# Optimization experiments

Measured on AMD Instinct MI355X. Metric: run time of the kernel, lower is better.

## Reference

```python
import jax, jax.numpy as jnp
import numpy as np

B, HIST, PRED = 16, 336, 48
S = HIST + PRED                      # 384 = max_seq_length
H, NL, NH, FF = 768, 12, 12, 3072    # default BertConfig
SA_NH = 16                           # attention_heads arg for the extra SelfAttention
V = 40000                            # num_location_ids
NE = 8                               # num_experts
D_DAY, D_TIME, D_DOW, D_WD, D_LOC = 64, 64, 64, 32, 256
D_IN = D_DAY + D_TIME + D_DOW + D_WD + D_LOC + 1  # 481


def _ln(x, g, b, eps):
    m = jnp.mean(x, -1, keepdims=True)
    v = jnp.mean(jnp.square(x - m), -1, keepdims=True)
    return (x - m) * jax.lax.rsqrt(v + eps) * g + b


def _mha(x, qW, qb, kW, kb, vW, vb, nh):
    b_, s_, h_ = x.shape
    hd = h_ // nh
    q = (x @ qW + qb).reshape(b_, s_, nh, hd)
    k = (x @ kW + kb).reshape(b_, s_, nh, hd)
    v = (x @ vW + vb).reshape(b_, s_, nh, hd)
    scores = jnp.einsum('bqhd,bkhd->bhqk', q, k) / jnp.sqrt(jnp.float32(hd))
    probs = jax.nn.softmax(scores, axis=-1)
    return jnp.einsum('bhqk,bkhd->bqhd', probs, v).reshape(b_, s_, h_)


FLOAT_NAMES = ['day_emb', 'time_emb', 'dow_emb', 'wd_emb', 'loc_emb',
               'ln_in_g', 'ln_in_b', 'inp_W', 'inp_b', 'res_W', 'res_b',
               'sa_qW', 'sa_qb', 'sa_kW', 'sa_kb', 'sa_vW', 'sa_vb', 'sa_oW', 'sa_ob', 'sa_lng', 'sa_lnb',
               'pos_emb', 'tt_emb', 'be_lng', 'be_lnb',
               'bqW', 'bqb', 'bkW', 'bkb', 'bvW', 'bvb', 'boW', 'bob', 'balng', 'balnb',
               'bf1W', 'bf1b', 'bf2W', 'bf2b', 'bflng', 'bflnb',
               'moe_W', 'moe_b', 'gate_W', 'gate_b', 'out_W', 'out_b']


def _forward(floats, ints):
    (day_emb, time_emb, dow_emb, wd_emb, loc_emb,
     ln_in_g, ln_in_b, inp_W, inp_b, res_W, res_b,
     sa_qW, sa_qb, sa_kW, sa_kb, sa_vW, sa_vb, sa_oW, sa_ob, sa_lng, sa_lnb,
     pos_emb, tt_emb, be_lng, be_lnb,
     bqW, bqb, bkW, bkb, bvW, bvb, boW, bob, balng, balnb,
     bf1W, bf1b, bf2W, bf2b, bflng, bflnb,
     moe_W, moe_b, gate_W, gate_b, out_W, out_b) = floats
    isf, hloc, psf = ints

    def feat(f):
        return (day_emb[f[:, :, 0]], time_emb[f[:, :, 1]], dow_emb[f[:, :, 3]],
                wd_emb[f[:, :, 4]], f[:, :, 5].astype(jnp.float32)[..., None])
    hd_, ht_, hw_, hwd_, hdl = feat(isf)
    hist = jnp.concatenate([hd_, ht_, hw_, hwd_, hdl, loc_emb[hloc]], -1)
    fd_, ft_, fw_, fwd_, fdl = feat(psf)
    fut_loc = jnp.zeros((psf.shape[0], psf.shape[1], D_LOC), jnp.float32)  # unknown future locations
    fut = jnp.concatenate([fd_, ft_, fw_, fwd_, fdl, fut_loc], -1)
    x = jnp.concatenate([hist, fut], 1)            # [B,S,481]
    x = _ln(x, ln_in_g, ln_in_b, 1e-5)             # layer_norm on raw features (dropout = identity in eval)
    proj = x @ inp_W + inp_b                       # input_projection -> [B,S,768]
    res = x @ res_W + res_b                        # residual_fc -> [B,S,768]

    # extra SelfAttention block (16 heads) with post-LN residual
    ctx = _mha(proj, sa_qW, sa_qb, sa_kW, sa_kb, sa_vW, sa_vb, SA_NH)
    h = _ln(ctx @ sa_oW + sa_ob + proj, sa_lng, sa_lnb, 1e-5)

    # BERT encoder (inputs_embeds path): add position + token_type(0) embeddings, then 12 post-LN layers
    h = _ln(h + pos_emb[None] + tt_emb, be_lng, be_lnb, 1e-12)
    for i in range(NL):
        ctx = _mha(h, bqW[i], bqb[i], bkW[i], bkb[i], bvW[i], bvb[i], NH)
        a = _ln(ctx @ boW[i] + bob[i] + h, balng[i], balnb[i], 1e-12)
        ff = jax.nn.gelu(a @ bf1W[i] + bf1b[i], approximate=False) @ bf2W[i] + bf2b[i]
        h = _ln(ff + a, bflng[i], bflnb[i], 1e-12)

    # dense soft-MoE: every expert runs on every token, softmax-gated sum
    xf = h.reshape(-1, H)                                                 # [B*S, H]
    eo = jax.nn.gelu(jnp.einsum('nd,edh->neh', xf, moe_W) + moe_b[None], approximate=False)
    gp = jax.nn.softmax(xf @ gate_W + gate_b, axis=-1)                     # [B*S, E]
    moe_out = jnp.einsum('ne,neh->nh', gp, eo).reshape(h.shape)

    logits = (moe_out + res) @ out_W + out_b                               # [B,S,V]
    return logits[:, HIST:, :]                                             # predictions for future slots


def setup_inputs() -> dict:
    key = jax.random.key(0)
    ctr = [0]
    def nk():
        ctr[0] += 1
        return jax.random.fold_in(key, ctr[0])
    def nrm(shape, s=0.02):
        return jax.random.normal(nk(), shape, jnp.float32) * s
    p = {}
    p['input_seq_feature'] = jax.random.randint(nk(), (B, HIST, 6), 0, 2)
    p['historical_locations'] = jax.random.randint(nk(), (B, HIST), 0, V)
    p['predict_seq_feature'] = jax.random.randint(nk(), (B, PRED, 6), 0, 2)
    p['day_emb'] = nrm((75, D_DAY)); p['time_emb'] = nrm((48, D_TIME))
    p['dow_emb'] = nrm((7, D_DOW)); p['wd_emb'] = nrm((2, D_WD)); p['loc_emb'] = nrm((V, D_LOC))
    p['ln_in_g'] = jnp.ones((D_IN,), jnp.float32); p['ln_in_b'] = jnp.zeros((D_IN,), jnp.float32)
    p['inp_W'] = nrm((D_IN, H)); p['inp_b'] = jnp.zeros((H,), jnp.float32)
    p['res_W'] = nrm((D_IN, H)); p['res_b'] = jnp.zeros((H,), jnp.float32)
    for n in ['sa_qW', 'sa_kW', 'sa_vW', 'sa_oW']:
        p[n] = nrm((H, H))
    for n in ['sa_qb', 'sa_kb', 'sa_vb', 'sa_ob']:
        p[n] = jnp.zeros((H,), jnp.float32)
    p['sa_lng'] = jnp.ones((H,), jnp.float32); p['sa_lnb'] = jnp.zeros((H,), jnp.float32)
    p['pos_emb'] = nrm((S, H)); p['tt_emb'] = nrm((H,))
    p['be_lng'] = jnp.ones((H,), jnp.float32); p['be_lnb'] = jnp.zeros((H,), jnp.float32)
    for n in ['bqW', 'bkW', 'bvW', 'boW']:
        p[n] = nrm((NL, H, H))
    for n in ['bqb', 'bkb', 'bvb', 'bob']:
        p[n] = jnp.zeros((NL, H), jnp.float32)
    p['balng'] = jnp.ones((NL, H), jnp.float32); p['balnb'] = jnp.zeros((NL, H), jnp.float32)
    p['bf1W'] = nrm((NL, H, FF)); p['bf1b'] = jnp.zeros((NL, FF), jnp.float32)
    p['bf2W'] = nrm((NL, FF, H)); p['bf2b'] = jnp.zeros((NL, H), jnp.float32)
    p['bflng'] = jnp.ones((NL, H), jnp.float32); p['bflnb'] = jnp.zeros((NL, H), jnp.float32)
    p['moe_W'] = nrm((NE, H, H)); p['moe_b'] = jnp.zeros((NE, H), jnp.float32)
    p['gate_W'] = nrm((H, NE)); p['gate_b'] = jnp.zeros((NE,), jnp.float32)
    p['out_W'] = nrm((H, V)); p['out_b'] = jnp.zeros((V,), jnp.float32)
    return p


def reference(input_seq_feature, historical_locations, predict_seq_feature,
              day_emb, time_emb, dow_emb, wd_emb, loc_emb,
              ln_in_g, ln_in_b, inp_W, inp_b, res_W, res_b,
              sa_qW, sa_qb, sa_kW, sa_kb, sa_vW, sa_vb, sa_oW, sa_ob, sa_lng, sa_lnb,
              pos_emb, tt_emb, be_lng, be_lnb,
              bqW, bqb, bkW, bkb, bvW, bvb, boW, bob, balng, balnb,
              bf1W, bf1b, bf2W, bf2b, bflng, bflnb,
              moe_W, moe_b, gate_W, gate_b, out_W, out_b):
    floats = (day_emb, time_emb, dow_emb, wd_emb, loc_emb,
              ln_in_g, ln_in_b, inp_W, inp_b, res_W, res_b,
              sa_qW, sa_qb, sa_kW, sa_kb, sa_vW, sa_vb, sa_oW, sa_ob, sa_lng, sa_lnb,
              pos_emb, tt_emb, be_lng, be_lnb,
              bqW, bqb, bkW, bkb, bvW, bvb, boW, bob, balng, balnb,
              bf1W, bf1b, bf2W, bf2b, bflng, bflnb,
              moe_W, moe_b, gate_W, gate_b, out_W, out_b)
    ints = (input_seq_feature, historical_locations, predict_seq_feature)
    return _forward(floats, ints)
```

## Files before the change

### kernel.cpp

```cpp
#include <hip/hip_runtime.h>
#include <cstddef>
#include <math.h>

#define BB 16
#define HIST 336
#define PRED 48
#define SS 384
#define HH 768
#define NL 12
#define FF_ 3072
#define DIN 481
#define DINP 512
#define NE_ 8
#define VV 40000
#define VVP 40064

typedef __attribute__((ext_vector_type(8))) short short8;
typedef __attribute__((ext_vector_type(4))) float f32x4;
struct short4v { short x, y, z, w; };

__device__ __forceinline__ short f2bf(float f) {
    union { float f; unsigned u; } v; v.f = f;
    unsigned r = v.u + 0x7fff + ((v.u >> 16) & 1);
    return (short)(r >> 16);
}

using gvoid_t = const __attribute__((address_space(1))) void;
using svoid_t = __attribute__((address_space(3))) void;

template<int OP>
__global__ __launch_bounds__(256)
void gemm_bf16(const short* __restrict__ A, const short* __restrict__ Bt,
               const float* __restrict__ bias, const float* __restrict__ bias2,
               const float* __restrict__ bias3,
               void* __restrict__ Cout, void* __restrict__ Cout2,
               int Kp, int M, int ldc)
{
    __shared__ short As[2][128 * 64];
    __shared__ short Bs[2][128 * 64];
    const int tid  = threadIdx.x;
    const int lane = tid & 63;
    const int w    = tid >> 6;
    const int wr = w >> 1, wc = w & 1;
    const int lrow = lane & 15, lgrp = lane >> 4;
    const size_t rowBase = (size_t)blockIdx.y * 128;
    const size_t colBase = (size_t)blockIdx.x * 128;

    f32x4 acc[4][4];
    #pragma unroll
    for (int i = 0; i < 4; ++i)
        #pragma unroll
        for (int j = 0; j < 4; ++j)
            acc[i][j] = f32x4{0.f, 0.f, 0.f, 0.f};

    const int nkt = Kp >> 6;

    auto stage = [&](int buf, int kt) {
        const short* Ab = A  + rowBase * Kp + (size_t)kt * 64;
        const short* Bb = Bt + colBase * Kp + (size_t)kt * 64;
        #pragma unroll
        for (int c = 0; c < 4; ++c) {
            const int sidx = (w * 4 + c) * 64 + lane;
            const int r = sidx >> 3, sl = sidx & 7;
            const int sseg = sl ^ (r & 7);
            __builtin_amdgcn_global_load_lds(
                (gvoid_t*)(Ab + (size_t)r * Kp + sseg * 8),
                (svoid_t*)&As[buf][(w * 4 + c) * 512], 16, 0, 0);
            __builtin_amdgcn_global_load_lds(
                (gvoid_t*)(Bb + (size_t)r * Kp + sseg * 8),
                (svoid_t*)&Bs[buf][(w * 4 + c) * 512], 16, 0, 0);
        }
    };

    int cur = 0;
    stage(0, 0);
    __syncthreads();
    for (int kt = 0; kt < nkt; ++kt) {
        if (kt + 1 < nkt) stage(cur ^ 1, kt + 1);
        const short* as = As[cur];
        const short* bs = Bs[cur];
        #pragma unroll
        for (int kk = 0; kk < 2; ++kk) {
            short8 aF[4], bF[4];
            #pragma unroll
            for (int mi = 0; mi < 4; ++mi) {
                const int r = wr * 64 + mi * 16 + lrow;
                const int seg = (kk * 4 + lgrp) ^ (r & 7);
                aF[mi] = *(const short8*)&as[r * 64 + seg * 8];
            }
            #pragma unroll
            for (int ni = 0; ni < 4; ++ni) {
                const int r = wc * 64 + ni * 16 + lrow;
                const int seg = (kk * 4 + lgrp) ^ (r & 7);
                bF[ni] = *(const short8*)&bs[r * 64 + seg * 8];
            }
            #pragma unroll
            for (int mi = 0; mi < 4; ++mi)
                #pragma unroll
                for (int ni = 0; ni < 4; ++ni)
                    acc[mi][ni] = __builtin_amdgcn_mfma_f32_16x16x32_bf16(
                        aF[mi], bF[ni], acc[mi][ni], 0, 0, 0);
        }
        __syncthreads();
        cur ^= 1;
    }

    #pragma unroll
    for (int mi = 0; mi < 4; ++mi) {
        #pragma unroll
        for (int ni = 0; ni < 4; ++ni) {
            const int col = (int)colBase + wc * 64 + ni * 16 + lrow;
            if (col >= M) continue;
            const float* bp = bias; int bc = col;
            if (bias2 && col >= HH) {
                if (col < 2 * HH) { bp = bias2; bc = col - HH; }
                else              { bp = bias3; bc = col - 2 * HH; }
            }
            const float bz = bp[bc];
            #pragma unroll
            for (int j = 0; j < 4; ++j) {
                const size_t row = rowBase + wr * 64 + mi * 16 + lgrp * 4 + j;
                float v = acc[mi][ni][j] + bz;
                if (OP == 1 || OP == 4)
                    v = 0.5f * v * (1.f + erff(v * 0.70710678118654752f));
                if (OP == 4 || OP == 5) ((short*)Cout)[row * ldc + col] = f2bf(v);
                else                    ((float*)Cout)[row * ldc + col] = v;
                if (OP == 6)            ((short*)Cout2)[row * ldc + col] = f2bf(v);
            }
        }
    }
}

template<int HD>
__global__ __launch_bounds__(256)
void attn_mfma(const short* __restrict__ Qg, const short* __restrict__ Kg,
               const short* __restrict__ Vg, short* __restrict__ Og,
               int nh, int ldq, int ldo, float scale)
{
    constexpr int NI = HD / 16;
    constexpr int SEGS = HD / 8;
    __shared__ short Qs[64 * 64];
    __shared__ short Ks[64 * 64];
    __shared__ short Vt[64 * 72];
    __shared__ short Ps[4][16 * 80];
    int idx = blockIdx.x;
    const int qt = idx % 6; idx /= 6;
    const int h = idx % nh; idx /= nh;
    const int b = idx;
    const int tid = threadIdx.x;
    const int lane = tid & 63;
    const int w = tid >> 6;
    const int lrow = lane & 15, lgrp = lane >> 4;

    const short* Qbase = Qg + ((size_t)(b * SS + qt * 64)) * ldq + h * HD;
    #pragma unroll
    for (int t = 0; t < 2; ++t) {
        const int i = tid + t * 256;
        const int r = i >> 3, sg = i & 7;
        short8 v = {0, 0, 0, 0, 0, 0, 0, 0};
        if (sg < SEGS) v = *(const short8*)(Qbase + (size_t)r * ldq + sg * 8);
        *(short8*)&Qs[r * 64 + (sg ^ (r & 7)) * 8] = v;
    }

    float m_[4], l_[4];
    f32x4 o_[NI];
    #pragma unroll
    for (int j = 0; j < 4; ++j) { m_[j] = -1e30f; l_[j] = 0.f; }
    #pragma unroll
    for (int ni = 0; ni < NI; ++ni) o_[ni] = f32x4{0.f, 0.f, 0.f, 0.f};

    for (int kt = 0; kt < 6; ++kt) {
        const short* Kb2 = Kg + ((size_t)(b * SS + kt * 64)) * ldq + h * HD;
        const short* Vb2 = Vg + ((size_t)(b * SS + kt * 64)) * ldq + h * HD;
        __syncthreads();
        #pragma unroll
        for (int c = 0; c < 2; ++c) {
            const int r = (w * 2 + c) * 8 + (lane >> 3);
            const int sg = (lane & 7) ^ (r & 7);
            __builtin_amdgcn_global_load_lds(
                (gvoid_t*)(Kb2 + (size_t)r * ldq + sg * 8),
                (svoid_t*)&Ks[(w * 2 + c) * 512], 16, 0, 0);
        }
        for (int i = tid; i < 64 * SEGS; i += 256) {
            const int k = i & 63, sg = i >> 6;
            short8 v = *(const short8*)(Vb2 + (size_t)k * ldq + sg * 8);
            #pragma unroll
            for (int j2 = 0; j2 < 8; ++j2)
                Vt[(sg * 8 + j2) * 72 + k] = v[j2];
        }
        __syncthreads();

        f32x4 s[4];
        #pragma unroll
        for (int ni = 0; ni < 4; ++ni) s[ni] = f32x4{0.f, 0.f, 0.f, 0.f};
        #pragma unroll
        for (int kk = 0; kk < 2; ++kk) {
            const int ra = w * 16 + lrow;
            const short8 aF = *(const short8*)&Qs[ra * 64 + ((kk * 4 + lgrp) ^ (ra & 7)) * 8];
            #pragma unroll
            for (int ni = 0; ni < 4; ++ni) {
                const int rb = ni * 16 + lrow;
                const short8 bF = *(const short8*)&Ks[rb * 64 + ((kk * 4 + lgrp) ^ (rb & 7)) * 8];
                s[ni] = __builtin_amdgcn_mfma_f32_16x16x32_bf16(aF, bF, s[ni], 0, 0, 0);
            }
        }
        #pragma unroll
        for (int ni = 0; ni < 4; ++ni)
            #pragma unroll
            for (int j = 0; j < 4; ++j) s[ni][j] *= scale;

        #pragma unroll
        for (int j = 0; j < 4; ++j) {
            float tm = fmaxf(fmaxf(s[0][j], s[1][j]), fmaxf(s[2][j], s[3][j]));
            #pragma unroll
            for (int d = 1; d < 16; d <<= 1) tm = fmaxf(tm, __shfl_xor(tm, d));
            const float mn = fmaxf(m_[j], tm);
            const float r2 = __expf(m_[j] - mn);
            float p[4], ps = 0.f;
            #pragma unroll
            for (int ni = 0; ni < 4; ++ni) { p[ni] = __expf(s[ni][j] - mn); ps += p[ni]; }
            #pragma unroll
            for (int d = 1; d < 16; d <<= 1) ps += __shfl_xor(ps, d);
            l_[j] = l_[j] * r2 + ps;
            m_[j] = mn;
            #pragma unroll
            for (int ni = 0; ni < NI; ++ni) o_[ni][j] *= r2;
            #pragma unroll
            for (int ni = 0; ni < 4; ++ni)
                Ps[w][(lgrp * 4 + j) * 80 + ni * 16 + lrow] = f2bf(p[ni]);
        }

        #pragma unroll
        for (int kk = 0; kk < 2; ++kk) {
            const short8 aP = *(const short8*)&Ps[w][lrow * 80 + kk * 32 + lgrp * 8];
            #pragma unroll
            for (int ni = 0; ni < NI; ++ni) {
                const int d0 = ni * 16 + lrow;
                const short8 bV = *(const short8*)&Vt[d0 * 72 + (kk * 4 + lgrp) * 8];
                o_[ni] = __builtin_amdgcn_mfma_f32_16x16x32_bf16(aP, bV, o_[ni], 0, 0, 0);
            }
        }
    }

    const size_t orow0 = (size_t)(b * SS + qt * 64 + w * 16);
    #pragma unroll
    for (int j = 0; j < 4; ++j) {
        const float inv = 1.f / l_[j];
        #pragma unroll
        for (int ni = 0; ni < NI; ++ni)
            Og[(orow0 + lgrp * 4 + j) * ldo + h * HD + ni * 16 + lrow] =
                f2bf(o_[ni][j] * inv);
    }
}

__global__ __launch_bounds__(256)
void transpose_cvt_b(const float* __restrict__ W, short* __restrict__ Wt,
                     int K, int M, int Kp, size_t sStride, size_t dStride)
{
    __shared__ float tile[32][33];
    const float* src = W + blockIdx.z * sStride;
    short* dst = Wt + blockIdx.z * dStride;
    const int m0 = blockIdx.x * 32, k0 = blockIdx.y * 32;
    const int tx = threadIdx.x, ty = threadIdx.y;
    #pragma unroll
    for (int i = 0; i < 4; ++i) {
        int k = k0 + ty + i * 8, m = m0 + tx;
        tile[ty + i * 8][tx] = (k < K && m < M) ? src[(size_t)k * M + m] : 0.f;
    }
    __syncthreads();
    #pragma unroll
    for (int i = 0; i < 4; ++i) {
        int m = m0 + ty + i * 8, k = k0 + tx;
        dst[(size_t)m * Kp + k] = f2bf(tile[tx][ty + i * 8]);
    }
}

__global__ __launch_bounds__(256)
void prep_layer_w(const float* __restrict__ bq, const float* __restrict__ bk,
                  const float* __restrict__ bv, const float* __restrict__ bo,
                  const float* __restrict__ f1, const float* __restrict__ f2,
                  short* __restrict__ qkvT, short* __restrict__ oT,
                  short* __restrict__ f1T, short* __restrict__ f2T)
{
    __shared__ float tile[32][33];
    int id = blockIdx.x;
    const float* src; short* dst; int K, M, tm, tk;
    if (id < 1728) {
        const int mat = id / 576, r = id % 576;
        src = mat == 0 ? bq : (mat == 1 ? bk : bv);
        dst = qkvT + (size_t)mat * HH * HH;
        K = HH; M = HH; tm = r % 24; tk = r / 24;
    } else if (id < 2304) {
        const int r = id - 1728;
        src = bo; dst = oT; K = HH; M = HH; tm = r % 24; tk = r / 24;
    } else if (id < 4608) {
        const int r = id - 2304;
        src = f1; dst = f1T; K = HH; M = FF_; tm = r % 96; tk = r / 96;
    } else {
        const int r = id - 4608;
        src = f2; dst = f2T; K = FF_; M = HH; tm = r % 24; tk = r / 24;
    }
    const int m0 = tm * 32, k0 = tk * 32;
    const int tx = threadIdx.x & 31, ty = threadIdx.x >> 5;
    #pragma unroll
    for (int i = 0; i < 4; ++i) {
        int k = k0 + ty + i * 8, m = m0 + tx;
        tile[ty + i * 8][tx] = src[(size_t)k * M + m];
    }
    __syncthreads();
    #pragma unroll
    for (int i = 0; i < 4; ++i) {
        int m = m0 + ty + i * 8, k = k0 + tx;
        dst[(size_t)m * K + k] = f2bf(tile[tx][ty + i * 8]);
    }
}

__global__ __launch_bounds__(256)
void cvt_bf16(const float* __restrict__ src, short* __restrict__ dst, int n4)
{
    int i = blockIdx.x * 256 + threadIdx.x;
    if (i >= n4) return;
    float4 v = reinterpret_cast<const float4*>(src)[i];
    short4v o = { f2bf(v.x), f2bf(v.y), f2bf(v.z), f2bf(v.w) };
    reinterpret_cast<short4v*>(dst)[i] = o;
}

__global__ __launch_bounds__(512)
void build_x(const int* __restrict__ isf, const int* __restrict__ hloc,
             const int* __restrict__ psf,
             const float* __restrict__ dayE, const float* __restrict__ timeE,
             const float* __restrict__ dowE, const float* __restrict__ wdE,
             const float* __restrict__ locE,
             const float* __restrict__ g, const float* __restrict__ b2,
             short* __restrict__ xb)
{
    const int tok = blockIdx.x;
    const int b = tok / SS, s = tok % SS;
    const int tid = threadIdx.x;
    __shared__ float red[512];
    const int* f;
    int loc = -1;
    if (s < HIST) { f = isf + (b * HIST + s) * 6; loc = hloc[b * HIST + s]; }
    else          { f = psf + (b * PRED + (s - HIST)) * 6; }
    float val = 0.f;
    if (tid < DIN) {
        int c = tid;
        if      (c < 64)  val = dayE[f[0] * 64 + c];
        else if (c < 128) val = timeE[f[1] * 64 + (c - 64)];
        else if (c < 192) val = dowE[f[3] * 64 + (c - 128)];
        else if (c < 224) val = wdE[f[4] * 32 + (c - 192)];
        else if (c == 224) val = (float)f[5];
        else val = (loc >= 0) ? locE[(size_t)loc * 256 + (c - 225)] : 0.f;
    }
    red[tid] = (tid < DIN) ? val : 0.f;
    __syncthreads();
    for (int o = 256; o > 0; o >>= 1) { if (tid < o) red[tid] += red[tid + o]; __syncthreads(); }
    float mean = red[0] / (float)DIN;
    __syncthreads();
    float d = (tid < DIN) ? (val - mean) : 0.f;
    red[tid] = d * d;
    __syncthreads();
    for (int o = 256; o > 0; o >>= 1) { if (tid < o) red[tid] += red[tid + o]; __syncthreads(); }
    float rstd = rsqrtf(red[0] / (float)DIN + 1e-5f);
    if (tid < DINP)
        xb[(size_t)tok * DINP + tid] =
            (tid < DIN) ? f2bf((val - mean) * rstd * g[tid] + b2[tid]) : (short)0;
}

__global__ __launch_bounds__(256)
void ln768(float* __restrict__ out, short* __restrict__ outb,
           const float* __restrict__ in1, const float* __restrict__ in2,
           const float* __restrict__ pos, const float* __restrict__ tt,
           const float* __restrict__ g, const float* __restrict__ b2,
           float eps)
{
    const int D = HH;
    const int row = blockIdx.x;
    const int s = row % SS;
    __shared__ float buf[HH];
    __shared__ float red[256];
    const int tid = threadIdx.x;
    float partial = 0.f;
    #pragma unroll
    for (int i = 0; i < 3; ++i) {
        int c = tid + i * 256;
        float v = in1[(size_t)row * D + c];
        if (in2) v += in2[(size_t)row * D + c];
        if (pos) v += pos[(size_t)s * D + c];
        if (tt)  v += tt[c];
        buf[c] = v;
        partial += v;
    }
    red[tid] = partial; __syncthreads();
    for (int o = 128; o > 0; o >>= 1) { if (tid < o) red[tid] += red[tid + o]; __syncthreads(); }
    float mean = red[0] / (float)D;
    __syncthreads();
    float p2 = 0.f;
    #pragma unroll
    for (int i = 0; i < 3; ++i) { float d = buf[tid + i * 256] - mean; p2 += d * d; }
    red[tid] = p2; __syncthreads();
    for (int o = 128; o > 0; o >>= 1) { if (tid < o) red[tid] += red[tid + o]; __syncthreads(); }
    float rstd = rsqrtf(red[0] / (float)D + eps);
    #pragma unroll
    for (int i = 0; i < 3; ++i) {
        int c = tid + i * 256;
        float v = (buf[c] - mean) * rstd * g[c] + b2[c];
        out[(size_t)row * D + c] = v;
        if (outb) outb[(size_t)row * D + c] = f2bf(v);
    }
}

__global__ void gather_fut_f32(const float* __restrict__ src, float* __restrict__ dst, int D)
{
    const int r = blockIdx.x;
    const int b = r / PRED, t = r % PRED;
    const int srow = b * SS + HIST + t;
    for (int c = threadIdx.x; c < D; c += blockDim.x)
        dst[(size_t)r * D + c] = src[(size_t)srow * D + c];
}
__global__ void gather_fut_b16(const short* __restrict__ src, short* __restrict__ dst, int D)
{
    const int r = blockIdx.x;
    const int b = r / PRED, t = r % PRED;
    const int srow = b * SS + HIST + t;
    for (int c = threadIdx.x; c < D; c += blockDim.x)
        dst[(size_t)r * D + c] = src[(size_t)srow * D + c];
}

__global__ __launch_bounds__(256)
void gate_kernel(const float* __restrict__ Xf, const float* __restrict__ Wg,
                 const float* __restrict__ bg, float* __restrict__ out)
{
    const int row = blockIdx.x;
    const int tid = threadIdx.x;
    float a[NE_] = {};
    for (int k = tid; k < HH; k += 256) {
        float xv = Xf[(size_t)row * HH + k];
        #pragma unroll
        for (int e = 0; e < NE_; ++e) a[e] = fmaf(xv, Wg[k * NE_ + e], a[e]);
    }
    __shared__ float red[256];
    #pragma unroll
    for (int e = 0; e < NE_; ++e) {
        red[tid] = a[e]; __syncthreads();
        for (int o = 128; o > 0; o >>= 1) { if (tid < o) red[tid] += red[tid + o]; __syncthreads(); }
        if (tid == 0) out[(size_t)row * NE_ + e] = red[0] + bg[e];
        __syncthreads();
    }
}

__global__ void gate_softmax(float* __restrict__ gate)
{
    const int r = blockIdx.x * blockDim.x + threadIdx.x;
    if (r >= BB * PRED) return;
    float* p = gate + (size_t)r * NE_;
    float mx = p[0];
    for (int e = 1; e < NE_; ++e) mx = fmaxf(mx, p[e]);
    float s = 0.f, v[NE_];
    for (int e = 0; e < NE_; ++e) { v[e] = __expf(p[e] - mx); s += v[e]; }
    for (int e = 0; e < NE_; ++e) p[e] = v[e] / s;
}

__global__ __launch_bounds__(256)
void moe_reduce(const float* __restrict__ eo, const float* __restrict__ gp,
                float* __restrict__ futm)
{
    const int row = blockIdx.x;
    float g[NE_];
    #pragma unroll
    for (int e = 0; e < NE_; ++e) g[e] = gp[row * NE_ + e];
    for (int c = threadIdx.x; c < HH; c += 256) {
        float s = futm[(size_t)row * HH + c];
        #pragma unroll
        for (int e = 0; e < NE_; ++e)
            s = fmaf(g[e], eo[(size_t)row * (NE_ * HH) + e * HH + c], s);
        futm[(size_t)row * HH + c] = s;
    }
}

extern "C" void kernel_launch(void* const* d_in, const int* in_sizes, int n_in,
                              void* d_out, int out_size, void* d_ws, size_t ws_size,
                              hipStream_t stream)
{
    const int*   isf   = (const int*)  d_in[0];
    const int*   hloc  = (const int*)  d_in[1];
    const int*   psf   = (const int*)  d_in[2];
    const float* dayE  = (const float*)d_in[3];
    const float* timeE = (const float*)d_in[4];
    const float* dowE  = (const float*)d_in[5];
    const float* wdE   = (const float*)d_in[6];
    const float* locE  = (const float*)d_in[7];
    const float* ln_g  = (const float*)d_in[8];
    const float* ln_b  = (const float*)d_in[9];
    const float* inpW  = (const float*)d_in[10];
    const float* inpB  = (const float*)d_in[11];
    const float* resW  = (const float*)d_in[12];
    const float* resB  = (const float*)d_in[13];
    const float* saqW  = (const float*)d_in[14];
    const float* sakW  = (const float*)d_in[15];
    const float* savW  = (const float*)d_in[16];
    const float* saoW  = (const float*)d_in[17];
    const float* saqB  = (const float*)d_in[18];
    const float* sakB  = (const float*)d_in[19];
    const float* savB  = (const float*)d_in[20];
    const float* saoB  = (const float*)d_in[21];
    const float* salnG = (const float*)d_in[22];
    const float* salnB = (const float*)d_in[23];
    const float* posE  = (const float*)d_in[24];
    const float* ttE   = (const float*)d_in[25];
    const float* belnG = (const float*)d_in[26];
    const float* belnB = (const float*)d_in[27];
    const float* bqW   = (const float*)d_in[28];
    const float* bkW   = (const float*)d_in[29];
    const float* bvW   = (const float*)d_in[30];
    const float* boW   = (const float*)d_in[31];
    const float* bqB   = (const float*)d_in[32];
    const float* bkB   = (const float*)d_in[33];
    const float* bvB   = (const float*)d_in[34];
    const float* boB   = (const float*)d_in[35];
    const float* balnG = (const float*)d_in[36];
    const float* balnB = (const float*)d_in[37];
    const float* bf1W  = (const float*)d_in[38];
    const float* bf1B  = (const float*)d_in[39];
    const float* bf2W  = (const float*)d_in[40];
    const float* bf2B  = (const float*)d_in[41];
    const float* bflnG = (const float*)d_in[42];
    const float* bflnB = (const float*)d_in[43];
    const float* moeW  = (const float*)d_in[44];
    const float* moeB  = (const float*)d_in[45];
    const float* gateW = (const float*)d_in[46];
    const float* gateB = (const float*)d_in[47];
    const float* outW  = (const float*)d_in[48];
    const float* outB  = (const float*)d_in[49];

    const int N6 = BB * SS;
    const int NF = BB * PRED;

    char* base = (char*)d_ws;
    size_t off = 0;
    auto alloc = [&](size_t bytes) -> void* {
        void* p = base + off;
        off = (off + bytes + 255) & ~(size_t)255;
        return p;
    };

    short* xb     = (short*)alloc((size_t)N6 * DINP * 2);
    short* hb     = (short*)alloc((size_t)N6 * HH * 2);
    short* Ob     = (short*)alloc((size_t)N6 * HH * 2);
    short* QKVb   = (short*)alloc((size_t)N6 * 3 * HH * 2);
    float* Cb     = (float*)alloc((size_t)N6 * HH * 4);
    short* ffb    = (short*)alloc((size_t)N6 * FF_ * 2);
    float* Hh     = (float*)alloc((size_t)N6 * HH * 4);
    float* Abuf   = (float*)alloc((size_t)N6 * HH * 4);
    short* inpWt  = (short*)alloc((size_t)HH * DINP * 2);
    short* resWt  = (short*)alloc((size_t)HH * DINP * 2);
    short* saWt   = (short*)alloc((size_t)3 * HH * HH * 2);
    short* saoWt  = (short*)alloc((size_t)HH * HH * 2);
    short* lqkvWt = (short*)alloc((size_t)3 * HH * HH * 2);
    short* loWt   = (short*)alloc((size_t)HH * HH * 2);
    short* lf1Wt  = (short*)alloc((size_t)FF_ * HH * 2);
    short* lf2Wt  = (short*)alloc((size_t)HH * FF_ * 2);
    float* futh   = (float*)alloc((size_t)NF * HH * 4);
    float* futm   = (float*)alloc((size_t)NF * HH * 4);
    float* futg   = (float*)alloc((size_t)NF * NE_ * 4);

    short* outWt = QKVb;
    short* moeWt = outWt + (size_t)VVP * HH;
    short* futhb = moeWt + (size_t)NE_ * HH * HH;
    short* futxb = futhb + (size_t)NF * HH;
    short* futmb = futxb + (size_t)NF * DINP;

    build_x<<<N6, 512, 0, stream>>>(isf, hloc, psf, dayE, timeE, dowE, wdE, locE,
                                    ln_g, ln_b, xb);

    dim3 tb(32, 8);
    transpose_cvt_b<<<dim3(HH/32, DINP/32, 1), tb, 0, stream>>>(inpW, inpWt, DIN, HH, DINP, 0, 0);
    transpose_cvt_b<<<dim3(HH/32, DINP/32, 1), tb, 0, stream>>>(resW, resWt, DIN, HH, DINP, 0, 0);
    transpose_cvt_b<<<dim3(HH/32, HH/32, 1), tb, 0, stream>>>(saqW, saWt,                   HH, HH, HH, 0, 0);
    transpose_cvt_b<<<dim3(HH/32, HH/32, 1), tb, 0, stream>>>(sakW, saWt + (size_t)HH*HH,   HH, HH, HH, 0, 0);
    transpose_cvt_b<<<dim3(HH/32, HH/32, 1), tb, 0, stream>>>(savW, saWt + (size_t)2*HH*HH, HH, HH, HH, 0, 0);
    transpose_cvt_b<<<dim3(HH/32, HH/32, 1), tb, 0, stream>>>(saoW, saoWt, HH, HH, HH, 0, 0);

    gemm_bf16<6><<<dim3(HH/128, N6/128), 256, 0, stream>>>(
        xb, inpWt, inpB, nullptr, nullptr, Abuf, hb, DINP, HH, HH);

    gemm_bf16<5><<<dim3(3*HH/128, N6/128), 256, 0, stream>>>(
        hb, saWt, saqB, sakB, savB, QKVb, nullptr, HH, 3*HH, 3*HH);
    attn_mfma<48><<<BB*16*6, 256, 0, stream>>>(
        QKVb, QKVb + HH, QKVb + 2*HH, Ob, 16, 3*HH, HH, 1.f / sqrtf(48.f));
    gemm_bf16<0><<<dim3(HH/128, N6/128), 256, 0, stream>>>(
        Ob, saoWt, saoB, nullptr, nullptr, Cb, nullptr, HH, HH, HH);
    ln768<<<N6, 256, 0, stream>>>(Hh, nullptr, Cb, Abuf, nullptr, nullptr,
                                  salnG, salnB, 1e-5f);

    ln768<<<N6, 256, 0, stream>>>(Hh, hb, Hh, nullptr, posE, ttE,
                                  belnG, belnB, 1e-12f);

    for (int i = 0; i < NL; ++i) {
        const size_t wo = (size_t)i * HH * HH;
        const size_t bo = (size_t)i * HH;
        prep_layer_w<<<6912, 256, 0, stream>>>(
            bqW + wo, bkW + wo, bvW + wo, boW + wo,
            bf1W + (size_t)i * HH * FF_, bf2W + (size_t)i * FF_ * HH,
            lqkvWt, loWt, lf1Wt, lf2Wt);

        gemm_bf16<5><<<dim3(3*HH/128, N6/128), 256, 0, stream>>>(
            hb, lqkvWt, bqB + bo, bkB + bo, bvB + bo, QKVb, nullptr, HH, 3*HH, 3*HH);
        attn_mfma<64><<<BB*12*6, 256, 0, stream>>>(
            QKVb, QKVb + HH, QKVb + 2*HH, Ob, 12, 3*HH, HH, 0.125f);
        gemm_bf16<0><<<dim3(HH/128, N6/128), 256, 0, stream>>>(
            Ob, loWt, boB + bo, nullptr, nullptr, Cb, nullptr, HH, HH, HH);
        ln768<<<N6, 256, 0, stream>>>(Abuf, hb, Cb, Hh, nullptr, nullptr,
                                      balnG + bo, balnB + bo, 1e-12f);
        gemm_bf16<4><<<dim3(FF_/128, N6/128), 256, 0, stream>>>(
            hb, lf1Wt, bf1B + (size_t)i * FF_, nullptr, nullptr, ffb, nullptr, HH, FF_, FF_);
        gemm_bf16<0><<<dim3(HH/128, N6/128), 256, 0, stream>>>(
            ffb, lf2Wt, bf2B + bo, nullptr, nullptr, Cb, nullptr, FF_, HH, HH);
        ln768<<<N6, 256, 0, stream>>>(Hh, hb, Cb, Abuf, nullptr, nullptr,
                                      bflnG + bo, bflnB + bo, 1e-12f);
    }

    gather_fut_f32<<<NF, 256, 0, stream>>>(Hh, futh, HH);
    gather_fut_b16<<<NF, 256, 0, stream>>>(hb, futhb, HH);
    gather_fut_b16<<<NF, 256, 0, stream>>>(xb, futxb, DINP);

    gemm_bf16<0><<<dim3(HH/128, NF/128), 256, 0, stream>>>(
        futxb, resWt, resB, nullptr, nullptr, futm, nullptr, DINP, HH, HH);

    gate_kernel<<<NF, 256, 0, stream>>>(futh, gateW, gateB, futg);
    gate_softmax<<<3, 256, 0, stream>>>(futg);

    transpose_cvt_b<<<dim3(HH/32, HH/32, NE_), tb, 0, stream>>>(
        moeW, moeWt, HH, HH, HH, (size_t)HH*HH, (size_t)HH*HH);
    gemm_bf16<1><<<dim3(NE_*HH/128, NF/128), 256, 0, stream>>>(
        futhb, moeWt, moeB, nullptr, nullptr, Hh, nullptr, HH, NE_*HH, NE_*HH);
    moe_reduce<<<NF, 256, 0, stream>>>(Hh, futg, futm);

    {
        int n4 = (int)((size_t)NF * HH / 4);
        cvt_bf16<<<(n4 + 255) / 256, 256, 0, stream>>>(futm, futmb, n4);
    }
    transpose_cvt_b<<<dim3(VVP/32, HH/32, 1), tb, 0, stream>>>(
        outW, outWt, HH, VV, HH, 0, 0);
    gemm_bf16<0><<<dim3(VVP/128, NF/128), 256, 0, stream>>>(
        futmb, outWt, outB, nullptr, nullptr, (float*)d_out, nullptr, HH, VV, VV);
}
```

Measured before the change: 3.735 ms.

## Swizzle GEMM blocks across XCDs, raise MFMA priority, warp-per-row layernorm

Adds an optional XCD-aware block remapping to the GEMM. It is enabled only for the MoE GEMM and the large vocabulary output GEMM, so that neighbouring tiles land on the same XCD and share its L2. The attention kernel gets s_setprio raised around its MFMA sections. The layernorm is rewritten to handle one row per wavefront with float4 loads and shuffle reductions, which removes the shared-memory tree reductions and barriers. The changes are small and mostly independent; the swizzle depends on the grid size dividing evenly and only helps if L2 locality was a bottleneck.

```diff
diff --git a/kernel.cpp b/kernel.cpp
--- a/kernel.cpp
+++ b/kernel.cpp
@@ -28,7 +28,7 @@
 using gvoid_t = const __attribute__((address_space(1))) void;
 using svoid_t = __attribute__((address_space(3))) void;
 
-template<int OP>
+template<int OP, bool SWZ>
 __global__ __launch_bounds__(256)
 void gemm_bf16(const short* __restrict__ A, const short* __restrict__ Bt,
                const float* __restrict__ bias, const float* __restrict__ bias2,
@@ -43,8 +43,19 @@
     const int w    = tid >> 6;
     const int wr = w >> 1, wc = w & 1;
     const int lrow = lane & 15, lgrp = lane >> 4;
-    const size_t rowBase = (size_t)blockIdx.y * 128;
-    const size_t colBase = (size_t)blockIdx.x * 128;
+
+    int bx = blockIdx.x, by = blockIdx.y;
+    if (SWZ) {
+        const int nwg = gridDim.x * gridDim.y;
+        const int o = blockIdx.y * gridDim.x + blockIdx.x;
+        const int xcd = o & 7, k = o >> 3;
+        const int q = nwg >> 3, r = nwg & 7;
+        const int nid = (xcd < r ? xcd * (q + 1) : r * (q + 1) + (xcd - r) * q) + k;
+        bx = nid / gridDim.y;
+        by = nid % gridDim.y;
+    }
+    const size_t rowBase = (size_t)by * 128;
+    const size_t colBase = (size_t)bx * 128;
 
     f32x4 acc[4][4];
     #pragma unroll
@@ -193,6 +204,7 @@
         f32x4 s[4];
         #pragma unroll
         for (int ni = 0; ni < 4; ++ni) s[ni] = f32x4{0.f, 0.f, 0.f, 0.f};
+        __builtin_amdgcn_s_setprio(1);
         #pragma unroll
         for (int kk = 0; kk < 2; ++kk) {
             const int ra = w * 16 + lrow;
@@ -204,6 +216,7 @@
                 s[ni] = __builtin_amdgcn_mfma_f32_16x16x32_bf16(aF, bF, s[ni], 0, 0, 0);
             }
         }
+        __builtin_amdgcn_s_setprio(0);
         #pragma unroll
         for (int ni = 0; ni < 4; ++ni)
             #pragma unroll
@@ -230,6 +243,7 @@
                 Ps[w][(lgrp * 4 + j) * 80 + ni * 16 + lrow] = f2bf(p[ni]);
         }
 
+        __builtin_amdgcn_s_setprio(1);
         #pragma unroll
         for (int kk = 0; kk < 2; ++kk) {
             const short8 aP = *(const short8*)&Ps[w][lrow * 80 + kk * 32 + lgrp * 8];
@@ -240,6 +254,7 @@
                 o_[ni] = __builtin_amdgcn_mfma_f32_16x16x32_bf16(aP, bV, o_[ni], 0, 0, 0);
             }
         }
+        __builtin_amdgcn_s_setprio(0);
     }
 
     const size_t orow0 = (size_t)(b * SS + qt * 64 + w * 16);
@@ -368,45 +383,57 @@
 }
 
 __global__ __launch_bounds__(256)
-void ln768(float* __restrict__ out, short* __restrict__ outb,
-           const float* __restrict__ in1, const float* __restrict__ in2,
-           const float* __restrict__ pos, const float* __restrict__ tt,
-           const float* __restrict__ g, const float* __restrict__ b2,
-           float eps)
-{
-    const int D = HH;
-    const int row = blockIdx.x;
+void ln768w(float* __restrict__ out, short* __restrict__ outb,
+            const float* __restrict__ in1, const float* __restrict__ in2,
+            const float* __restrict__ pos, const float* __restrict__ tt,
+            const float* __restrict__ g, const float* __restrict__ b2,
+            float eps)
+{
+    const int w = threadIdx.x >> 6, lane = threadIdx.x & 63;
+    const int row = blockIdx.x * 4 + w;
     const int s = row % SS;
-    __shared__ float buf[HH];
-    __shared__ float red[256];
-    const int tid = threadIdx.x;
+    float4 v[3];
     float partial = 0.f;
     #pragma unroll
     for (int i = 0; i < 3; ++i) {
-        int c = tid + i * 256;
-        float v = in1[(size_t)row * D + c];
-        if (in2) v += in2[(size_t)row * D + c];
-        if (pos) v += pos[(size_t)s * D + c];
-        if (tt)  v += tt[c];
-        buf[c] = v;
-        partial += v;
-    }
-    red[tid] = partial; __syncthreads();
-    for (int o = 128; o > 0; o >>= 1) { if (tid < o) red[tid] += red[tid + o]; __syncthreads(); }
-    float mean = red[0] / (float)D;
-    __syncthreads();
+        const int c = i * 256 + lane * 4;
+        float4 t = *(const float4*)&in1[(size_t)row * HH + c];
+        if (in2) { float4 u = *(const float4*)&in2[(size_t)row * HH + c];
+                   t.x += u.x; t.y += u.y; t.z += u.z; t.w += u.w; }
+        if (pos) { float4 u = *(const float4*)&pos[(size_t)s * HH + c];
+                   t.x += u.x; t.y += u.y; t.z += u.z; t.w += u.w; }
+        if (tt)  { float4 u = *(const float4*)&tt[c];
+                   t.x += u.x; t.y += u.y; t.z += u.z; t.w += u.w; }
+        v[i] = t;
+        partial += t.x + t.y + t.z + t.w;
+    }
+    #pragma unroll
+    for (int d = 1; d < 64; d <<= 1) partial += __shfl_xor(partial, d);
+    const float mean = partial * (1.f / 768.f);
     float p2 = 0.f;
     #pragma unroll
-    for (int i = 0; i < 3; ++i) { float d = buf[tid + i * 256] - mean; p2 += d * d; }
-    red[tid] = p2; __syncthreads();
-    for (int o = 128; o > 0; o >>= 1) { if (tid < o) red[tid] += red[tid + o]; __syncthreads(); }
-    float rstd = rsqrtf(red[0] / (float)D + eps);
-    #pragma unroll
     for (int i = 0; i < 3; ++i) {
-        int c = tid + i * 256;
-        float v = (buf[c] - mean) * rstd * g[c] + b2[c];
-        out[(size_t)row * D + c] = v;
-        if (outb) outb[(size_t)row * D + c] = f2bf(v);
+        float a = v[i].x - mean, b3 = v[i].y - mean, c3 = v[i].z - mean, d3 = v[i].w - mean;
+        p2 += a * a + b3 * b3 + c3 * c3 + d3 * d3;
+    }
+    #pragma unroll
+    for (int d = 1; d < 64; d <<= 1) p2 += __shfl_xor(p2, d);
+    const float rstd = rsqrtf(p2 * (1.f / 768.f) + eps);
+    #pragma unroll
+    for (int i = 0; i < 3; ++i) {
+        const int c = i * 256 + lane * 4;
+        float4 gg = *(const float4*)&g[c];
+        float4 bb = *(const float4*)&b2[c];
+        float4 o;
+        o.x = (v[i].x - mean) * rstd * gg.x + bb.x;
+        o.y = (v[i].y - mean) * rstd * gg.y + bb.y;
+        o.z = (v[i].z - mean) * rstd * gg.z + bb.z;
+        o.w = (v[i].w - mean) * rstd * gg.w + bb.w;
+        *(float4*)&out[(size_t)row * HH + c] = o;
+        if (outb) {
+            short4v ob = { f2bf(o.x), f2bf(o.y), f2bf(o.z), f2bf(o.w) };
+            *(short4v*)&outb[(size_t)row * HH + c] = ob;
+        }
     }
 }
 
@@ -581,20 +608,20 @@
     transpose_cvt_b<<<dim3(HH/32, HH/32, 1), tb, 0, stream>>>(savW, saWt + (size_t)2*HH*HH, HH, HH, HH, 0, 0);
     transpose_cvt_b<<<dim3(HH/32, HH/32, 1), tb, 0, stream>>>(saoW, saoWt, HH, HH, HH, 0, 0);
 
-    gemm_bf16<6><<<dim3(HH/128, N6/128), 256, 0, stream>>>(
+    gemm_bf16<6, false><<<dim3(HH/128, N6/128), 256, 0, stream>>>(
         xb, inpWt, inpB, nullptr, nullptr, Abuf, hb, DINP, HH, HH);
 
-    gemm_bf16<5><<<dim3(3*HH/128, N6/128), 256, 0, stream>>>(
+    gemm_bf16<5, false><<<dim3(3*HH/128, N6/128), 256, 0, stream>>>(
         hb, saWt, saqB, sakB, savB, QKVb, nullptr, HH, 3*HH, 3*HH);
     attn_mfma<48><<<BB*16*6, 256, 0, stream>>>(
         QKVb, QKVb + HH, QKVb + 2*HH, Ob, 16, 3*HH, HH, 1.f / sqrtf(48.f));
-    gemm_bf16<0><<<dim3(HH/128, N6/128), 256, 0, stream>>>(
+    gemm_bf16<0, false><<<dim3(HH/128, N6/128), 256, 0, stream>>>(
         Ob, saoWt, saoB, nullptr, nullptr, Cb, nullptr, HH, HH, HH);
-    ln768<<<N6, 256, 0, stream>>>(Hh, nullptr, Cb, Abuf, nullptr, nullptr,
-                                  salnG, salnB, 1e-5f);
-
-    ln768<<<N6, 256, 0, stream>>>(Hh, hb, Hh, nullptr, posE, ttE,
-                                  belnG, belnB, 1e-12f);
+    ln768w<<<N6/4, 256, 0, stream>>>(Hh, nullptr, Cb, Abuf, nullptr, nullptr,
+                                     salnG, salnB, 1e-5f);
+
+    ln768w<<<N6/4, 256, 0, stream>>>(Hh, hb, Hh, nullptr, posE, ttE,
+                                     belnG, belnB, 1e-12f);
 
     for (int i = 0; i < NL; ++i) {
         const size_t wo = (size_t)i * HH * HH;
@@ -604,27 +631,27 @@
             bf1W + (size_t)i * HH * FF_, bf2W + (size_t)i * FF_ * HH,
             lqkvWt, loWt, lf1Wt, lf2Wt);
 
-        gemm_bf16<5><<<dim3(3*HH/128, N6/128), 256, 0, stream>>>(
+        gemm_bf16<5, false><<<dim3(3*HH/128, N6/128), 256, 0, stream>>>(
             hb, lqkvWt, bqB + bo, bkB + bo, bvB + bo, QKVb, nullptr, HH, 3*HH, 3*HH);
         attn_mfma<64><<<BB*12*6, 256, 0, stream>>>(
             QKVb, QKVb + HH, QKVb + 2*HH, Ob, 12, 3*HH, HH, 0.125f);
-        gemm_bf16<0><<<dim3(HH/128, N6/128), 256, 0, stream>>>(
+        gemm_bf16<0, false><<<dim3(HH/128, N6/128), 256, 0, stream>>>(
             Ob, loWt, boB + bo, nullptr, nullptr, Cb, nullptr, HH, HH, HH);
-        ln768<<<N6, 256, 0, stream>>>(Abuf, hb, Cb, Hh, nullptr, nullptr,
-                                      balnG + bo, balnB + bo, 1e-12f);
-        gemm_bf16<4><<<dim3(FF_/128, N6/128), 256, 0, stream>>>(
+        ln768w<<<N6/4, 256, 0, stream>>>(Abuf, hb, Cb, Hh, nullptr, nullptr,
+                                         balnG + bo, balnB + bo, 1e-12f);
+        gemm_bf16<4, false><<<dim3(FF_/128, N6/128), 256, 0, stream>>>(
             hb, lf1Wt, bf1B + (size_t)i * FF_, nullptr, nullptr, ffb, nullptr, HH, FF_, FF_);
-        gemm_bf16<0><<<dim3(HH/128, N6/128), 256, 0, stream>>>(
+        gemm_bf16<0, false><<<dim3(HH/128, N6/128), 256, 0, stream>>>(
             ffb, lf2Wt, bf2B + bo, nullptr, nullptr, Cb, nullptr, FF_, HH, HH);
-        ln768<<<N6, 256, 0, stream>>>(Hh, hb, Cb, Abuf, nullptr, nullptr,
-                                      bflnG + bo, bflnB + bo, 1e-12f);
+        ln768w<<<N6/4, 256, 0, stream>>>(Hh, hb, Cb, Abuf, nullptr, nullptr,
+                                         bflnG + bo, bflnB + bo, 1e-12f);
     }
 
     gather_fut_f32<<<NF, 256, 0, stream>>>(Hh, futh, HH);
     gather_fut_b16<<<NF, 256, 0, stream>>>(hb, futhb, HH);
     gather_fut_b16<<<NF, 256, 0, stream>>>(xb, futxb, DINP);
 
-    gemm_bf16<0><<<dim3(HH/128, NF/128), 256, 0, stream>>>(
+    gemm_bf16<0, false><<<dim3(HH/128, NF/128), 256, 0, stream>>>(
         futxb, resWt, resB, nullptr, nullptr, futm, nullptr, DINP, HH, HH);
 
     gate_kernel<<<NF, 256, 0, stream>>>(futh, gateW, gateB, futg);
@@ -632,7 +659,7 @@
 
     transpose_cvt_b<<<dim3(HH/32, HH/32, NE_), tb, 0, stream>>>(
         moeW, moeWt, HH, HH, HH, (size_t)HH*HH, (size_t)HH*HH);
-    gemm_bf16<1><<<dim3(NE_*HH/128, NF/128), 256, 0, stream>>>(
+    gemm_bf16<1, true><<<dim3(NE_*HH/128, NF/128), 256, 0, stream>>>(
         futhb, moeWt, moeB, nullptr, nullptr, Hh, nullptr, HH, NE_*HH, NE_*HH);
     moe_reduce<<<NF, 256, 0, stream>>>(Hh, futg, futm);
 
@@ -642,6 +669,6 @@
     }
     transpose_cvt_b<<<dim3(VVP/32, HH/32, 1), tb, 0, stream>>>(
         outW, outWt, HH, VV, HH, 0, 0);
-    gemm_bf16<0><<<dim3(VVP/128, NF/128), 256, 0, stream>>>(
+    gemm_bf16<0, true><<<dim3(VVP/128, NF/128), 256, 0, stream>>>(
         futmb, outWt, outB, nullptr, nullptr, (float*)d_out, nullptr, HH, VV, VV);
 }
```

Result: faster. 3.633 ms (-2.7%).
